# Kernel tuning notes

Measured on AMD Instinct MI355X. Metric: run time of the kernel, lower is better.

## Reference

```python
import jax, jax.numpy as jnp
import numpy as np
import math

SEQ_LEN = 720
PRED_LEN = 720
CHANNELS = 862
BATCH = 64
IN_LEN = SEQ_LEN // 2  # seq_len is even -> no padding branch


def dct2_ortho_matrix(N):
    # Orthonormal DCT-II matrix D so that dct(x, norm='ortho') = x @ D.T along last axis
    n = jnp.arange(N, dtype=jnp.float32)
    k = n[:, None]
    D = jnp.cos(jnp.pi * (n[None, :] + 0.5) * k / N) * jnp.sqrt(2.0 / N)
    D = D.at[0].multiply(1.0 / jnp.sqrt(2.0))
    return D  # [N, N], row k = frequency k


def setup_inputs() -> dict:
    key = jax.random.key(0)
    ks = jax.random.split(key, 7)
    x = jax.random.normal(ks[0], (BATCH, SEQ_LEN, CHANNELS), dtype=jnp.float32)
    # depthwise 1x1 convs == per-channel scale + bias
    w1 = jax.random.normal(ks[1], (CHANNELS,), dtype=jnp.float32) * 0.1
    b1 = jax.random.normal(ks[2], (CHANNELS,), dtype=jnp.float32) * 0.1
    w2 = jax.random.normal(ks[3], (CHANNELS,), dtype=jnp.float32) * 0.1
    b2 = jax.random.normal(ks[4], (CHANNELS,), dtype=jnp.float32) * 0.1
    # Linear(in_len, pred_len): W [pred_len, in_len], b [pred_len]
    W_lo = jax.random.normal(ks[5], (PRED_LEN, IN_LEN), dtype=jnp.float32) / math.sqrt(IN_LEN)
    b_lo = jax.random.normal(ks[6], (PRED_LEN,), dtype=jnp.float32) * 0.01
    return {"x": x, "w1": w1, "b1": b1, "w2": w2, "b2": b2, "W_lo": W_lo, "b_lo": b_lo}


def reference(x, w1, b1, w2, b2, W_lo, b_lo):
    B, L, C = x.shape
    xt = jnp.transpose(x, (0, 2, 1))              # [B, C, L]
    seq_mean = jnp.mean(xt, axis=-1, keepdims=True)
    xt = xt - seq_mean
    # depthwise low-pass conv, kernel [1,1]/sqrt(2), stride 2
    lp = xt.reshape(B, C, L // 2, 2).sum(-1) / jnp.sqrt(jnp.float32(2.0))  # [B, C, N]
    N = L // 2
    D = dct2_ortho_matrix(N)
    xd = jnp.einsum('bcn,kn->bck', lp, D) / N     # DCT-II ortho along last axis, scaled
    # x += conv1x1_1(conv1x1_2(x)) -- depthwise 1x1 convs are per-channel affine
    y = (xd * w2[:, None] + b2[:, None]) * w1[:, None] + b1[:, None]
    xd = xd + y
    out = jnp.einsum('bcn,pn->bcp', xd, W_lo) + b_lo  # Linear(in_len -> pred_len)
    out = out + seq_mean                           # [B, C, pred_len]
    return jnp.transpose(out, (0, 2, 1))           # [B, pred_len, C]
```

## Files before the change

### kernel.cpp

```cpp
#include <hip/hip_runtime.h>
#include <hip/hip_bf16.h>
#include <cstdint>

#define SEQ   720
#define PRED  720
#define CH    862
#define NB    64
#define NIN   360
#define KP    384
#define CP    896
#define PP    768
#define BK    32

typedef __attribute__((ext_vector_type(8))) short s16x8;
typedef __attribute__((ext_vector_type(4))) float f32x4;
typedef __attribute__((ext_vector_type(2))) float f32x2;
typedef unsigned int u32;
typedef unsigned short u16;

__device__ __forceinline__ u16 to_bf16u(float f){
  __hip_bfloat16 h = __float2bfloat16(f);
  return *reinterpret_cast<u16*>(&h);
}

__global__ __launch_bounds__(256) void k_dct(float* __restrict__ Dm){
  int idx = blockIdx.x*256 + threadIdx.x;
  if (idx >= NIN*NIN) return;
  int n = idx / NIN, m = idx % NIN;
  int r = ((2*m+1)*n) % (4*NIN);
  float ang = (float)r * (float)(3.14159265358979323846 / 720.0);
  float v = cosf(ang) * 0.07453559924999299f;
  if (n == 0) v *= 0.7071067811865476f;
  Dm[idx] = v;
}

__global__ __launch_bounds__(384) void k_mmat(const float* __restrict__ Wlo, const float* __restrict__ Dm,
                                              u16* __restrict__ Mbf, float* __restrict__ Srow,
                                              float* __restrict__ Slo){
  int p = blockIdx.x;
  int t = threadIdx.x;
  if (p >= PRED){
    Mbf[(size_t)p*KP + t] = 0;
    if (t == 0){ Srow[p] = 0.f; Slo[p] = 0.f; }
    return;
  }
  __shared__ float Wrow[NIN];
  __shared__ float redM[6], redW[6];
  if (t < NIN) Wrow[t] = Wlo[(size_t)p*NIN + t];
  __syncthreads();
  float acc = 0.f;
  if (t < NIN){
    const float* Dc = Dm + t;
    #pragma unroll 4
    for (int n = 0; n < NIN; n++) acc += Wrow[n] * Dc[(size_t)n*NIN];
    acc *= (1.0f/360.0f);
  }
  Mbf[(size_t)p*KP + t] = (t < NIN) ? to_bf16u(acc) : (u16)0;
  float mv = (t < NIN) ? acc : 0.f;
  float wv = (t < NIN) ? Wrow[t] : 0.f;
  #pragma unroll
  for (int off = 32; off > 0; off >>= 1){
    mv += __shfl_down(mv, off);
    wv += __shfl_down(wv, off);
  }
  int wid = t >> 6, lid = t & 63;
  if (lid == 0){ redM[wid] = mv; redW[wid] = wv; }
  __syncthreads();
  if (t == 0){
    float sm = 0.f, sw = 0.f;
    #pragma unroll
    for (int i = 0; i < 6; i++){ sm += redM[i]; sw += redW[i]; }
    Srow[p] = sm; Slo[p] = sw;
  }
}

__global__ __launch_bounds__(256) void k_pre(const float* __restrict__ x, u16* __restrict__ pairB,
                                             float* __restrict__ meanw){
  int b  = blockIdx.y;
  int c0 = blockIdx.x * 64;
  int t  = threadIdx.x;
  int c16  = t & 15;
  int mrow = t >> 4;
  int w    = t >> 6;
  __shared__ u16  pl[192][66];
  __shared__ float red[4][64];
  const float rs2 = 0.7071067811865476f;
  int cb = c0 + c16*4;
  bool full = (cb + 3 < CH);
  const float* xb = x + (size_t)b*SEQ*CH + cb;
  float s0=0.f, s1=0.f, s2=0.f, s3=0.f;
  int rowc = t >> 2;
  int mq0  = t & 3;
  size_t rbase = ((size_t)b*CP + c0 + rowc) * KP;

  #pragma unroll 1
  for (int h = 0; h < 2; h++){
    #pragma unroll 1
    for (int ml = mrow; ml < 192; ml += 16){
      int m = h*192 + ml;
      float p0=0.f, p1=0.f, p2=0.f, p3=0.f;
      if (m < NIN){
        const float* r0 = xb + (size_t)(2*m)*CH;
        float a0,a1,a2,a3, e0,e1,e2,e3;
        if (full){
          f32x4 va = *reinterpret_cast<const f32x4*>(r0);
          f32x2 vb = *reinterpret_cast<const f32x2*>(r0 + CH);
          f32x2 vc = *reinterpret_cast<const f32x2*>(r0 + CH + 2);
          a0=va.x; a1=va.y; a2=va.z; a3=va.w;
          e0=vb.x; e1=vb.y; e2=vc.x; e3=vc.y;
        } else {
          a0 = (cb+0<CH)? r0[0]:0.f; a1 = (cb+1<CH)? r0[1]:0.f;
          a2 = (cb+2<CH)? r0[2]:0.f; a3 = (cb+3<CH)? r0[3]:0.f;
          e0 = (cb+0<CH)? r0[CH+0]:0.f; e1 = (cb+1<CH)? r0[CH+1]:0.f;
          e2 = (cb+2<CH)? r0[CH+2]:0.f; e3 = (cb+3<CH)? r0[CH+3]:0.f;
        }
        p0=a0+e0; p1=a1+e1; p2=a2+e2; p3=a3+e3;
        s0+=p0; s1+=p1; s2+=p2; s3+=p3;
      }
      u32 lo = (u32)to_bf16u(p0*rs2) | ((u32)to_bf16u(p1*rs2) << 16);
      u32 hi = (u32)to_bf16u(p2*rs2) | ((u32)to_bf16u(p3*rs2) << 16);
      *reinterpret_cast<u32*>(&pl[ml][c16*4 + 0]) = lo;
      *reinterpret_cast<u32*>(&pl[ml][c16*4 + 2]) = hi;
    }
    __syncthreads();
    #pragma unroll
    for (int i = 0; i < 6; i++){
      int mg = mq0 + 4*i;
      u16 vals[8];
      #pragma unroll
      for (int j = 0; j < 8; j++) vals[j] = pl[mg*8 + j][rowc];
      uint4 pk;
      pk.x = (u32)vals[0] | ((u32)vals[1] << 16);
      pk.y = (u32)vals[2] | ((u32)vals[3] << 16);
      pk.z = (u32)vals[4] | ((u32)vals[5] << 16);
      pk.w = (u32)vals[6] | ((u32)vals[7] << 16);
      *reinterpret_cast<uint4*>(pairB + rbase + h*192 + (size_t)mg*8) = pk;
    }
    __syncthreads();
  }

  s0 += __shfl_down(s0, 32); s1 += __shfl_down(s1, 32);
  s2 += __shfl_down(s2, 32); s3 += __shfl_down(s3, 32);
  s0 += __shfl_down(s0, 16); s1 += __shfl_down(s1, 16);
  s2 += __shfl_down(s2, 16); s3 += __shfl_down(s3, 16);
  if ((t & 63) < 16){
    f32x4 rv; rv.x=s0; rv.y=s1; rv.z=s2; rv.w=s3;
    *reinterpret_cast<f32x4*>(&red[w][c16*4]) = rv;
  }
  __syncthreads();
  if (t < 64){
    float mean = (red[0][t] + red[1][t] + red[2][t] + red[3][t]) * (1.0f/SEQ);
    meanw[(size_t)b*CP + c0 + t] = mean;
  }
}

#define GLOAD_LDS16(gp, lp_) __builtin_amdgcn_global_load_lds( \
    (const __attribute__((address_space(1))) u32*)(gp), \
    (__attribute__((address_space(3))) u32*)(lp_), 16, 0, 0)

__global__ __launch_bounds__(256, 4) void k_gemm(const u16* __restrict__ Apack, const u16* __restrict__ Mbf,
                                              const float* __restrict__ Srow, const float* __restrict__ Slo,
                                              const float* __restrict__ meanw,
                                              const float* __restrict__ w1, const float* __restrict__ b1,
                                              const float* __restrict__ w2, const float* __restrict__ b2,
                                              const float* __restrict__ blo,
                                              float* __restrict__ out){
  int bid = blockIdx.x;
  int idx = (bid & 7) * 336 + (bid >> 3);
  int pt  = idx % 6;
  int rem = idx / 6;
  int ct  = rem % 7;
  int b   = rem / 7;

  int t  = threadIdx.x;
  int w  = t >> 6, l = t & 63;
  int wr = w >> 1, wc = w & 1;

  __shared__ __align__(16) char smem[49152];
  u16 (*As)[128*BK] = reinterpret_cast<u16(*)[128*BK]>(smem);
  u16 (*Bs)[128*BK] = reinterpret_cast<u16(*)[128*BK]>(smem + 24576);
  float (*wbuf)[16][132] = reinterpret_cast<float(*)[16][132]>(smem);

  f32x4 acc[4][4] = {};

  const u16* Abase = Apack + ((size_t)b*CP + (size_t)ct*128) * KP;
  const u16* Bbase = Mbf + (size_t)pt*128*KP;
  int srow = t >> 2;
  int squad = t & 3;
  int row16 = l & 15, kb = l >> 4;
  int sperm = (srow >> 1) & 3;
  int rperm = (row16 >> 1) & 3;

#define STAGE(bufi, k0) do { \
    GLOAD_LDS16(Abase + (size_t)(srow)*KP + (k0) + ((squad^sperm))*8,      &As[bufi][(srow)*BK + squad*8]); \
    GLOAD_LDS16(Abase + (size_t)(64 + srow)*KP + (k0) + ((squad^sperm))*8, &As[bufi][(64 + srow)*BK + squad*8]); \
    GLOAD_LDS16(Bbase + (size_t)(srow)*KP + (k0) + ((squad^sperm))*8,      &Bs[bufi][(srow)*BK + squad*8]); \
    GLOAD_LDS16(Bbase + (size_t)(64 + srow)*KP + (k0) + ((squad^sperm))*8, &Bs[bufi][(64 + srow)*BK + squad*8]); \
  } while(0)

  STAGE(0, 0);
  STAGE(1, BK);
  for (int ks = 0; ks < 12; ks++){
    int cur = ks % 3;
    if (ks < 11){
      asm volatile("s_waitcnt vmcnt(4)" ::: "memory");
    } else {
      asm volatile("s_waitcnt vmcnt(0)" ::: "memory");
    }
    __builtin_amdgcn_s_barrier();
    if (ks < 10){
      STAGE((ks + 2) % 3, (ks + 2) * BK);
    }
    s16x8 af[4], bfr[4];
    #pragma unroll
    for (int mi = 0; mi < 4; mi++)
      af[mi] = *reinterpret_cast<const s16x8*>(&As[cur][(wr*64 + mi*16 + row16)*BK + (kb^rperm)*8]);
    #pragma unroll
    for (int ni = 0; ni < 4; ni++)
      bfr[ni] = *reinterpret_cast<const s16x8*>(&Bs[cur][(wc*64 + ni*16 + row16)*BK + (kb^rperm)*8]);
    __builtin_amdgcn_s_setprio(1);
    #pragma unroll
    for (int mi = 0; mi < 4; mi++)
      #pragma unroll
      for (int ni = 0; ni < 4; ni++)
        acc[mi][ni] = __builtin_amdgcn_mfma_f32_16x16x32_bf16(af[mi], bfr[ni], acc[mi][ni], 0, 0, 0);
    __builtin_amdgcn_s_setprio(0);
  }
  __syncthreads();

  int c32 = t & 31;
  int cb4 = ct*128 + c32*4;
  float sc4[4], of4[4], cn4[4], bc4[4];
  #pragma unroll
  for (int j = 0; j < 4; j++){
    int c = cb4 + j;
    bool v = (c < CH);
    float w1v = v ? w1[c] : 0.f, w2v = v ? w2[c] : 0.f;
    float b1v = v ? b1[c] : 0.f, b2v = v ? b2[c] : 0.f;
    float mv  = v ? meanw[(size_t)b*CP + c] : 0.f;
    sc4[j] = 1.f + w1v*w2v;
    of4[j] = w1v*b2v + b1v;
    cn4[j] = mv;
    bc4[j] = 1.4142135623730951f * sc4[j] * mv;
  }
  bool cfull = (cb4 + 3 < CH);
  size_t outb = (size_t)b*PRED*CH;
  int prow = t >> 5;

  #pragma unroll
  for (int ni = 0; ni < 4; ni++){
    #pragma unroll
    for (int mi = 0; mi < 4; mi++)
      #pragma unroll
      for (int r = 0; r < 4; r++)
        wbuf[wc][row16][wr*64 + mi*16 + kb*4 + r] = acc[mi][ni][r];
    __syncthreads();
    #pragma unroll
    for (int k = 0; k < 4; k++){
      int wcp   = k >> 1;
      int p_loc = (k & 1)*8 + prow;
      int p = pt*128 + wcp*64 + ni*16 + p_loc;
      if (p < PRED){
        f32x4 g = *reinterpret_cast<const f32x4*>(&wbuf[wcp][p_loc][c32*4]);
        float sp = Srow[p], sl = Slo[p], bl = blo[p];
        f32x4 ov;
        #pragma unroll
        for (int j = 0; j < 4; j++)
          ov[j] = sc4[j]*g[j] + (cn4[j] - bc4[j]*sp + of4[j]*sl + bl);
        float* op = &out[outb + (size_t)p*CH + cb4];
        if (cfull){
          *reinterpret_cast<f32x4*>(op) = ov;
        } else {
          #pragma unroll
          for (int j = 0; j < 4; j++)
            if (cb4 + j < CH) op[j] = ov[j];
        }
      }
    }
    __syncthreads();
  }
}

extern "C" void kernel_launch(void* const* d_in, const int* in_sizes, int n_in,
                              void* d_out, int out_size, void* d_ws, size_t ws_size,
                              hipStream_t stream)
{
  const float* x   = (const float*)d_in[0];
  const float* w1  = (const float*)d_in[1];
  const float* b1  = (const float*)d_in[2];
  const float* w2  = (const float*)d_in[3];
  const float* b2  = (const float*)d_in[4];
  const float* Wlo = (const float*)d_in[5];
  const float* blo = (const float*)d_in[6];
  float* out = (float*)d_out;

  char* ws = (char*)d_ws;
  float* Dm    = (float*)(ws);
  u16*   Mbf   = (u16*)(ws + 518400);
  float* Srow  = (float*)(ws + 518400 + 589824);
  float* Slo   = (float*)(ws + 518400 + 589824 + 3072);
  u16*   pairB = (u16*)(ws + 518400 + 589824 + 6144);
  float* meanw = (float*)(ws + 518400 + 589824 + 6144 + 44040192);

  k_dct<<<dim3((NIN*NIN + 255)/256), dim3(256), 0, stream>>>(Dm);
  k_mmat<<<dim3(PP), dim3(384), 0, stream>>>(Wlo, Dm, Mbf, Srow, Slo);
  k_pre<<<dim3(CP/64, NB), dim3(256), 0, stream>>>(x, pairB, meanw);
  k_gemm<<<dim3(6*7*NB), dim3(256), 0, stream>>>(pairB, Mbf, Srow, Slo, meanw,
                                                 w1, b1, w2, b2, blo, out);
}
```

Measured before the change: 156.2 us.

## Restructure GEMM to 128x64 tiles with full-K B in LDS and register-streamed A

The GEMM tile shrinks from 128x128 to 128 channels by 64 predictions, doubling the grid to 12 prediction tiles. The whole K-extent of the B (M matrix) tile is loaded into LDS once with an XOR swizzle, and the three-stage pipelined K-loop with barriers is gone. Each wave now reads its A fragments straight from global memory into registers with one-step prefetch, which removes per-iteration barriers and LDS staging for A. The cost is that A traffic is now uncoalesced global loads, re-read by twice as many blocks, and each wave does less MFMA work per B fragment.

```diff
diff --git a/kernel.cpp b/kernel.cpp
--- a/kernel.cpp
+++ b/kernel.cpp
@@ -10,7 +10,7 @@
 #define KP    384
 #define CP    896
 #define PP    768
-#define BK    32
+#define NPT   12
 
 typedef __attribute__((ext_vector_type(8))) short s16x8;
 typedef __attribute__((ext_vector_type(4))) float f32x4;
@@ -166,65 +166,63 @@
                                               const float* __restrict__ blo,
                                               float* __restrict__ out){
   int bid = blockIdx.x;
-  int idx = (bid & 7) * 336 + (bid >> 3);
-  int pt  = idx % 6;
-  int rem = idx / 6;
+  int idx = (bid & 7) * 672 + (bid >> 3);
+  int pt  = idx % NPT;
+  int rem = idx / NPT;
   int ct  = rem % 7;
   int b   = rem / 7;
 
-  int t  = threadIdx.x;
-  int w  = t >> 6, l = t & 63;
-  int wr = w >> 1, wc = w & 1;
-
-  __shared__ __align__(16) char smem[49152];
-  u16 (*As)[128*BK] = reinterpret_cast<u16(*)[128*BK]>(smem);
-  u16 (*Bs)[128*BK] = reinterpret_cast<u16(*)[128*BK]>(smem + 24576);
-  float (*wbuf)[16][132] = reinterpret_cast<float(*)[16][132]>(smem);
-
-  f32x4 acc[4][4] = {};
-
-  const u16* Abase = Apack + ((size_t)b*CP + (size_t)ct*128) * KP;
-  const u16* Bbase = Mbf + (size_t)pt*128*KP;
-  int srow = t >> 2;
-  int squad = t & 3;
+  int t = threadIdx.x;
+  int w = t >> 6, l = t & 63;
   int row16 = l & 15, kb = l >> 4;
-  int sperm = (srow >> 1) & 3;
-  int rperm = (row16 >> 1) & 3;
-
-#define STAGE(bufi, k0) do { \
-    GLOAD_LDS16(Abase + (size_t)(srow)*KP + (k0) + ((squad^sperm))*8,      &As[bufi][(srow)*BK + squad*8]); \
-    GLOAD_LDS16(Abase + (size_t)(64 + srow)*KP + (k0) + ((squad^sperm))*8, &As[bufi][(64 + srow)*BK + squad*8]); \
-    GLOAD_LDS16(Bbase + (size_t)(srow)*KP + (k0) + ((squad^sperm))*8,      &Bs[bufi][(srow)*BK + squad*8]); \
-    GLOAD_LDS16(Bbase + (size_t)(64 + srow)*KP + (k0) + ((squad^sperm))*8, &Bs[bufi][(64 + srow)*BK + squad*8]); \
-  } while(0)
-
-  STAGE(0, 0);
-  STAGE(1, BK);
+
+  __shared__ __align__(16) u16 Bs[64 * KP];
+  float (*wbuf)[132] = reinterpret_cast<float(*)[132]>(Bs);
+
+  const u16* Bbase = Mbf + (size_t)pt*64*KP;
+  #pragma unroll
+  for (int i = 0; i < 12; i++){
+    int id = i*256 + t;
+    int r  = id / 48;
+    int pc = id % 48;
+    int lc = (pc & ~7) | ((pc ^ r) & 7);
+    GLOAD_LDS16(Bbase + (size_t)r*KP + lc*8, Bs + id*8);
+  }
+  __syncthreads();
+
+  f32x4 acc[2][4] = {};
+  const u16* aptr = Apack + ((size_t)b*CP + ct*128 + w*32 + row16)*KP + kb*8;
+  int beven[4], bodd[4];
+  #pragma unroll
+  for (int nj = 0; nj < 4; nj++){
+    int r = nj*16 + row16;
+    beven[nj] = r*KP + ((kb       ^ r) & 7)*8;
+    bodd [nj] = r*KP + (((kb + 4) ^ r) & 7)*8;
+  }
+
+  s16x8 a0 = *reinterpret_cast<const s16x8*>(aptr);
+  s16x8 a1 = *reinterpret_cast<const s16x8*>(aptr + 16*KP);
+  #pragma unroll
   for (int ks = 0; ks < 12; ks++){
-    int cur = ks % 3;
+    s16x8 a0n, a1n;
     if (ks < 11){
-      asm volatile("s_waitcnt vmcnt(4)" ::: "memory");
-    } else {
-      asm volatile("s_waitcnt vmcnt(0)" ::: "memory");
-    }
-    __builtin_amdgcn_s_barrier();
-    if (ks < 10){
-      STAGE((ks + 2) % 3, (ks + 2) * BK);
-    }
-    s16x8 af[4], bfr[4];
-    #pragma unroll
-    for (int mi = 0; mi < 4; mi++)
-      af[mi] = *reinterpret_cast<const s16x8*>(&As[cur][(wr*64 + mi*16 + row16)*BK + (kb^rperm)*8]);
-    #pragma unroll
-    for (int ni = 0; ni < 4; ni++)
-      bfr[ni] = *reinterpret_cast<const s16x8*>(&Bs[cur][(wc*64 + ni*16 + row16)*BK + (kb^rperm)*8]);
+      a0n = *reinterpret_cast<const s16x8*>(aptr + (ks+1)*32);
+      a1n = *reinterpret_cast<const s16x8*>(aptr + 16*KP + (ks+1)*32);
+    }
+    s16x8 bfr[4];
+    #pragma unroll
+    for (int nj = 0; nj < 4; nj++){
+      int bix = ((ks & 1) ? bodd[nj] : beven[nj]) + (ks >> 1)*64;
+      bfr[nj] = *reinterpret_cast<const s16x8*>(&Bs[bix]);
+    }
     __builtin_amdgcn_s_setprio(1);
     #pragma unroll
-    for (int mi = 0; mi < 4; mi++)
+    for (int mi = 0; mi < 2; mi++)
       #pragma unroll
-      for (int ni = 0; ni < 4; ni++)
-        acc[mi][ni] = __builtin_amdgcn_mfma_f32_16x16x32_bf16(af[mi], bfr[ni], acc[mi][ni], 0, 0, 0);
+      for (int nj = 0; nj < 4; nj++)
+        acc[mi][nj] = __builtin_amdgcn_mfma_f32_16x16x32_bf16(mi ? a1 : a0, bfr[nj], acc[mi][nj], 0, 0, 0);
     __builtin_amdgcn_s_setprio(0);
+    a0 = a0n; a1 = a1n;
   }
   __syncthreads();
 
@@ -248,20 +246,19 @@
   int prow = t >> 5;
 
   #pragma unroll
-  for (int ni = 0; ni < 4; ni++){
-    #pragma unroll
-    for (int mi = 0; mi < 4; mi++)
+  for (int nj = 0; nj < 4; nj++){
+    #pragma unroll
+    for (int mi = 0; mi < 2; mi++)
       #pragma unroll
       for (int r = 0; r < 4; r++)
-        wbuf[wc][row16][wr*64 + mi*16 + kb*4 + r] = acc[mi][ni][r];
+        wbuf[row16][w*32 + mi*16 + kb*4 + r] = acc[mi][nj][r];
     __syncthreads();
     #pragma unroll
-    for (int k = 0; k < 4; k++){
-      int wcp   = k >> 1;
-      int p_loc = (k & 1)*8 + prow;
-      int p = pt*128 + wcp*64 + ni*16 + p_loc;
+    for (int k2 = 0; k2 < 2; k2++){
+      int p_loc = k2*8 + prow;
+      int p = pt*64 + nj*16 + p_loc;
       if (p < PRED){
-        f32x4 g = *reinterpret_cast<const f32x4*>(&wbuf[wcp][p_loc][c32*4]);
+        f32x4 g = *reinterpret_cast<const f32x4*>(&wbuf[p_loc][c32*4]);
         float sp = Srow[p], sl = Slo[p], bl = blo[p];
         f32x4 ov;
         #pragma unroll
@@ -305,6 +302,6 @@
   k_dct<<<dim3((NIN*NIN + 255)/256), dim3(256), 0, stream>>>(Dm);
   k_mmat<<<dim3(PP), dim3(384), 0, stream>>>(Wlo, Dm, Mbf, Srow, Slo);
   k_pre<<<dim3(CP/64, NB), dim3(256), 0, stream>>>(x, pairB, meanw);
-  k_gemm<<<dim3(6*7*NB), dim3(256), 0, stream>>>(pairB, Mbf, Srow, Slo, meanw,
-                                                 w1, b1, w2, b2, blo, out);
-}
+  k_gemm<<<dim3(NB*7*NPT), dim3(256), 0, stream>>>(pairB, Mbf, Srow, Slo, meanw,
+                                                   w1, b1, w2, b2, blo, out);
+}
```

Measured after the change: 193.6 us. 24.0% more time.
